# Performance work log

Measured on AMD Instinct MI355X. Metric: run time of the kernel, lower is better.

Reference implementation:

```python
import jax, jax.numpy as jnp
import numpy as np


def setup_inputs() -> dict:
    key = jax.random.key(0)
    B, U, I, H = 8192, 16, 128, 128
    k = jax.random.split(key, 6)
    s = 1.0 / np.sqrt(H)  # PyTorch GRU init scale (uniform(-s, s)); use scaled normal for test data
    return {
        "inputs": jax.random.normal(k[0], (B, U, I), dtype=jnp.float32),
        "hidden": jax.random.normal(k[1], (B, U, H), dtype=jnp.float32),
        "w_ih": jax.random.normal(k[2], (U, 3 * H, I), dtype=jnp.float32) * s,
        "w_hh": jax.random.normal(k[3], (U, 3 * H, H), dtype=jnp.float32) * s,
        "b_ih": jax.random.normal(k[4], (U, 3 * H), dtype=jnp.float32) * s,
        "b_hh": jax.random.normal(k[5], (U, 3 * H), dtype=jnp.float32) * s,
    }


def reference(inputs, hidden, w_ih, w_hh, b_ih, b_hh):
    # Grouped single-step GRU: one independent GRU cell per unit u, batched via einsum.
    # PyTorch GRU gate order in the 3H dim: [reset, update, new].
    H = hidden.shape[-1]
    # gates_x[b,u,g] = sum_i inputs[b,u,i] * w_ih[u,g,i] + b_ih[u,g]
    gx = jnp.einsum("bui,ugi->bug", inputs, w_ih) + b_ih  # (B, U, 3H)
    gh = jnp.einsum("buh,ugh->bug", hidden, w_hh) + b_hh  # (B, U, 3H)
    xr, xz, xn = gx[..., :H], gx[..., H:2 * H], gx[..., 2 * H:]
    hr, hz, hn = gh[..., :H], gh[..., H:2 * H], gh[..., 2 * H:]
    r = jax.nn.sigmoid(xr + hr)
    z = jax.nn.sigmoid(xz + hz)
    n = jnp.tanh(xn + r * hn)
    return (1.0 - z) * n + z * hidden  # (B, U, H)
```

## Files before the change

### kernel.cpp

```cpp
#include <hip/hip_runtime.h>
#include <hip/hip_bf16.h>

typedef __attribute__((ext_vector_type(8))) short  short8;
typedef __attribute__((ext_vector_type(4))) float  floatx4;

#define UH   2048
#define XPAD 264

#define MFMA16(a,b,c) __builtin_amdgcn_mfma_f32_16x16x32_bf16(a, b, c, 0, 0, 0)

static __device__ __forceinline__ unsigned int pkbf16(float a, float b) {
    __hip_bfloat162 p = __float22bfloat162_rn(make_float2(a, b));
    return *(unsigned int*)&p;
}

__global__ __launch_bounds__(256) void prep(const float* __restrict__ w_ih,
                                            const float* __restrict__ w_hh,
                                            const float* __restrict__ b_ih,
                                            const float* __restrict__ b_hh,
                                            __hip_bfloat16* __restrict__ Wc,
                                            float* __restrict__ bias_c) {
    if (blockIdx.x < 768) {
        int t   = blockIdx.x * 256 + threadIdx.x;
        int k8  = t & 31;
        int row = t >> 5;
        int u   = row / 384;
        int g   = row - u * 384;
        int k   = k8 * 8;
        const float* src = (k < 128) ? (w_ih + (size_t)row * 128 + k)
                                     : (w_hh + (size_t)row * 128 + (k - 128));
        float4 v0 = ((const float4*)src)[0];
        float4 v1 = ((const float4*)src)[1];
        uint4 w;
        w.x = pkbf16(v0.x, v0.y);
        w.y = pkbf16(v0.z, v0.w);
        w.z = pkbf16(v1.x, v1.y);
        w.w = pkbf16(v1.z, v1.w);
        int gt = g >> 4, lr = g & 15;
        int s  = k8 >> 2, lq = k8 & 3;
        size_t off = (size_t)((u * 24 + gt) * 8 + s) * 512 + (lq * 16 + lr) * 8;
        *(uint4*)(Wc + off) = w;
    } else {
        int idx = (blockIdx.x - 768) * 256 + threadIdx.x;
        int u = idx >> 9;
        int g = idx & 511;
        float v;
        if (g < 256)       v = b_ih[u * 384 + g] + b_hh[u * 384 + g];
        else if (g < 384)  v = b_ih[u * 384 + g];
        else               v = b_hh[u * 384 + (g - 128)];
        bias_c[idx] = v;
    }
}

__global__ __launch_bounds__(512, 3) void gru_fused(
    const float* __restrict__ inputs, const float* __restrict__ hidden,
    const __hip_bfloat16* __restrict__ Wc, const float* __restrict__ bias_c,
    float* __restrict__ out)
{
    __shared__ __align__(16) __hip_bfloat16 Xs[64][XPAD];
    __shared__ float bs[512];

    const int bx  = blockIdx.x;
    const int u   = ((bx & 7) << 1) | ((bx >> 3) & 1);
    const int mt  = bx >> 4;
    const int b0  = mt * 64;
    const int tid = threadIdx.x;

    bs[tid] = bias_c[u * 512 + tid];

    const float* xbase = inputs + (size_t)b0 * UH + u * 128;
    const float* hbase = hidden + (size_t)b0 * UH + u * 128;
    #pragma unroll
    for (int i = 0; i < 8; ++i) {
        int f   = i * 512 + tid;
        int row = f >> 6;
        int col = (f & 63) * 4;
        const float* src = (col < 128) ? (xbase + (size_t)row * UH + col)
                                       : (hbase + (size_t)row * UH + (col - 128));
        float4 v = *(const float4*)src;
        uint2 w;
        w.x = pkbf16(v.x, v.y);
        w.y = pkbf16(v.z, v.w);
        *(uint2*)&Xs[row][col] = w;
    }
    __syncthreads();

    const int lane = tid & 63;
    const int wv   = tid >> 6;
    const int lr   = lane & 15;
    const int lq   = lane >> 4;

    floatx4 aR[4], aZ[4], aXN[4], aHN[4];
    #pragma unroll
    for (int m4 = 0; m4 < 4; ++m4) {
        aR[m4]  = (floatx4){0.f, 0.f, 0.f, 0.f};
        aZ[m4]  = (floatx4){0.f, 0.f, 0.f, 0.f};
        aXN[m4] = (floatx4){0.f, 0.f, 0.f, 0.f};
        aHN[m4] = (floatx4){0.f, 0.f, 0.f, 0.f};
    }

    const short* WgU = (const short*)Wc + (size_t)u * 98304 + lane * 8;

    #pragma unroll
    for (int s = 0; s < 8; ++s) {
        short8 aF[4];
        #pragma unroll
        for (int m4 = 0; m4 < 4; ++m4)
            aF[m4] = *(const short8*)((const short*)&Xs[m4 * 16 + lr][0] + s * 32 + lq * 8);

        short8 bR = *(const short8*)(WgU + (size_t)(wv * 8 + s) * 512);
        short8 bZ = *(const short8*)(WgU + (size_t)(64 + wv * 8 + s) * 512);
        short8 bN = *(const short8*)(WgU + (size_t)(128 + wv * 8 + s) * 512);

        #pragma unroll
        for (int m4 = 0; m4 < 4; ++m4) {
            aR[m4] = MFMA16(aF[m4], bR, aR[m4]);
            aZ[m4] = MFMA16(aF[m4], bZ, aZ[m4]);
            if (s < 4) aXN[m4] = MFMA16(aF[m4], bN, aXN[m4]);
            else       aHN[m4] = MFMA16(aF[m4], bN, aHN[m4]);
        }
    }

    const int c = wv * 16 + lr;
    const float br  = bs[c];
    const float bz  = bs[128 + c];
    const float bxn = bs[256 + c];
    const float bhn = bs[384 + c];
    float* obase = out + (size_t)b0 * UH + u * 128 + c;

    #pragma unroll
    for (int m4 = 0; m4 < 4; ++m4) {
        #pragma unroll
        for (int r = 0; r < 4; ++r) {
            const int m = m4 * 16 + lq * 4 + r;
            float rv = __builtin_amdgcn_rcpf(1.f + __expf(-(aR[m4][r] + br)));
            float zv = __builtin_amdgcn_rcpf(1.f + __expf(-(aZ[m4][r] + bz)));
            float npre = (aXN[m4][r] + bxn) + rv * (aHN[m4][r] + bhn);
            float nv = 2.f * __builtin_amdgcn_rcpf(1.f + __expf(-2.f * npre)) - 1.f;
            float hv = __bfloat162float(Xs[m][128 + c]);
            obase[(size_t)m * UH] = nv + zv * (hv - nv);
        }
    }
}


extern "C" void kernel_launch(void* const* d_in, const int* in_sizes, int n_in,
                              void* d_out, int out_size, void* d_ws, size_t ws_size,
                              hipStream_t stream) {
    const float* inputs = (const float*)d_in[0];
    const float* hidden = (const float*)d_in[1];
    const float* w_ih   = (const float*)d_in[2];
    const float* w_hh   = (const float*)d_in[3];
    const float* b_ih   = (const float*)d_in[4];
    const float* b_hh   = (const float*)d_in[5];
    float* out = (float*)d_out;

    __hip_bfloat16* Wc = (__hip_bfloat16*)d_ws;
    float* bias_c = (float*)((char*)d_ws + (size_t)16 * 384 * 256 * 2);

    prep<<<dim3(800), dim3(256), 0, stream>>>(w_ih, w_hh, b_ih, b_hh, Wc, bias_c);
    gru_fused<<<dim3(2048), dim3(512), 0, stream>>>(inputs, hidden, Wc, bias_c, out);
}
```

Before: 200.0 us.

## Make GRU kernel persistent over 8 batch tiles with register-held weights and double buffering

```diff
diff --git a/kernel.cpp b/kernel.cpp
--- a/kernel.cpp
+++ b/kernel.cpp
@@ -52,93 +52,118 @@
     }
 }
 
-__global__ __launch_bounds__(512, 3) void gru_fused(
+__global__ __launch_bounds__(512, 2) void gru_fused(
     const float* __restrict__ inputs, const float* __restrict__ hidden,
     const __hip_bfloat16* __restrict__ Wc, const float* __restrict__ bias_c,
     float* __restrict__ out)
 {
-    __shared__ __align__(16) __hip_bfloat16 Xs[64][XPAD];
-    __shared__ float bs[512];
+    __shared__ __align__(16) __hip_bfloat16 Xs[2][64][XPAD];
 
-    const int bx  = blockIdx.x;
-    const int u   = ((bx & 7) << 1) | ((bx >> 3) & 1);
-    const int mt  = bx >> 4;
-    const int b0  = mt * 64;
-    const int tid = threadIdx.x;
-
-    bs[tid] = bias_c[u * 512 + tid];
-
-    const float* xbase = inputs + (size_t)b0 * UH + u * 128;
-    const float* hbase = hidden + (size_t)b0 * UH + u * 128;
-    #pragma unroll
-    for (int i = 0; i < 8; ++i) {
-        int f   = i * 512 + tid;
-        int row = f >> 6;
-        int col = (f & 63) * 4;
-        const float* src = (col < 128) ? (xbase + (size_t)row * UH + col)
-                                       : (hbase + (size_t)row * UH + (col - 128));
-        float4 v = *(const float4*)src;
-        uint2 w;
-        w.x = pkbf16(v.x, v.y);
-        w.y = pkbf16(v.z, v.w);
-        *(uint2*)&Xs[row][col] = w;
-    }
-    __syncthreads();
-
+    const int bx   = blockIdx.x;
+    const int u    = ((bx & 7) << 1) | ((bx >> 3) & 1);
+    const int mt0  = (bx >> 4) * 8;
+    const int tid  = threadIdx.x;
     const int lane = tid & 63;
     const int wv   = tid >> 6;
     const int lr   = lane & 15;
     const int lq   = lane >> 4;
 
-    floatx4 aR[4], aZ[4], aXN[4], aHN[4];
+    const short* WgU = (const short*)Wc + (size_t)u * 98304 + lane * 8;
+    short8 fR[8], fZ[8], fN[8];
     #pragma unroll
-    for (int m4 = 0; m4 < 4; ++m4) {
-        aR[m4]  = (floatx4){0.f, 0.f, 0.f, 0.f};
-        aZ[m4]  = (floatx4){0.f, 0.f, 0.f, 0.f};
-        aXN[m4] = (floatx4){0.f, 0.f, 0.f, 0.f};
-        aHN[m4] = (floatx4){0.f, 0.f, 0.f, 0.f};
+    for (int s = 0; s < 8; ++s) {
+        fR[s] = *(const short8*)(WgU + (size_t)(       wv * 8 + s) * 512);
+        fZ[s] = *(const short8*)(WgU + (size_t)( 64 +  wv * 8 + s) * 512);
+        fN[s] = *(const short8*)(WgU + (size_t)(128 +  wv * 8 + s) * 512);
     }
 
-    const short* WgU = (const short*)Wc + (size_t)u * 98304 + lane * 8;
+    const int   c   = wv * 16 + lr;
+    const float br  = bias_c[u * 512 + c];
+    const float bz  = bias_c[u * 512 + 128 + c];
+    const float bxn = bias_c[u * 512 + 256 + c];
+    const float bhn = bias_c[u * 512 + 384 + c];
 
-    #pragma unroll
-    for (int s = 0; s < 8; ++s) {
-        short8 aF[4];
+    const int scol = (tid & 63) * 4;
+    const float* sbase = ((scol < 128) ? (inputs + scol)
+                                       : (hidden + (scol - 128)))
+                       + (size_t)u * 128;
+
+    float4 stg[8];
+
+    auto ISSUE = [&](int mt) {
+        const float* p = sbase + (size_t)(mt * 64 + wv) * UH;
         #pragma unroll
-        for (int m4 = 0; m4 < 4; ++m4)
-            aF[m4] = *(const short8*)((const short*)&Xs[m4 * 16 + lr][0] + s * 32 + lq * 8);
+        for (int i = 0; i < 8; ++i)
+            stg[i] = *(const float4*)(p + (size_t)(i * 8) * UH);
+    };
+    auto WRITE = [&](int buf) {
+        #pragma unroll
+        for (int i = 0; i < 8; ++i) {
+            uint2 w;
+            w.x = pkbf16(stg[i].x, stg[i].y);
+            w.y = pkbf16(stg[i].z, stg[i].w);
+            *(uint2*)&Xs[buf][i * 8 + wv][scol] = w;
+        }
+    };
+    auto BARRIER = [&]() {
+        asm volatile("s_waitcnt lgkmcnt(0)" ::: "memory");
+        __builtin_amdgcn_sched_barrier(0);
+        __builtin_amdgcn_s_barrier();
+        __builtin_amdgcn_sched_barrier(0);
+    };
 
-        short8 bR = *(const short8*)(WgU + (size_t)(wv * 8 + s) * 512);
-        short8 bZ = *(const short8*)(WgU + (size_t)(64 + wv * 8 + s) * 512);
-        short8 bN = *(const short8*)(WgU + (size_t)(128 + wv * 8 + s) * 512);
+    ISSUE(mt0 + 0);
+    WRITE(0);
+    ISSUE(mt0 + 1);
+    BARRIER();
 
+    #pragma unroll 1
+    for (int j = 0; j < 8; ++j) {
+        const int buf = j & 1;
+
+        floatx4 aR[4], aZ[4], aXN[4], aHN[4];
         #pragma unroll
         for (int m4 = 0; m4 < 4; ++m4) {
-            aR[m4] = MFMA16(aF[m4], bR, aR[m4]);
-            aZ[m4] = MFMA16(aF[m4], bZ, aZ[m4]);
-            if (s < 4) aXN[m4] = MFMA16(aF[m4], bN, aXN[m4]);
-            else       aHN[m4] = MFMA16(aF[m4], bN, aHN[m4]);
+            aR[m4]  = (floatx4){0.f, 0.f, 0.f, 0.f};
+            aZ[m4]  = (floatx4){0.f, 0.f, 0.f, 0.f};
+            aXN[m4] = (floatx4){0.f, 0.f, 0.f, 0.f};
+            aHN[m4] = (floatx4){0.f, 0.f, 0.f, 0.f};
         }
-    }
+        #pragma unroll
+        for (int s = 0; s < 8; ++s) {
+            short8 aF[4];
+            #pragma unroll
+            for (int m4 = 0; m4 < 4; ++m4)
+                aF[m4] = *(const short8*)((const short*)&Xs[buf][m4 * 16 + lr][0]
+                                          + s * 32 + lq * 8);
+            #pragma unroll
+            for (int m4 = 0; m4 < 4; ++m4) {
+                aR[m4] = MFMA16(aF[m4], fR[s], aR[m4]);
+                aZ[m4] = MFMA16(aF[m4], fZ[s], aZ[m4]);
+                if (s < 4) aXN[m4] = MFMA16(aF[m4], fN[s], aXN[m4]);
+                else       aHN[m4] = MFMA16(aF[m4], fN[s], aHN[m4]);
+            }
+        }
 
-    const int c = wv * 16 + lr;
-    const float br  = bs[c];
-    const float bz  = bs[128 + c];
-    const float bxn = bs[256 + c];
-    const float bhn = bs[384 + c];
-    float* obase = out + (size_t)b0 * UH + u * 128 + c;
+        float* obase = out + (size_t)(mt0 + j) * 64 * UH + u * 128 + c;
+        #pragma unroll
+        for (int m4 = 0; m4 < 4; ++m4) {
+            #pragma unroll
+            for (int r = 0; r < 4; ++r) {
+                const int m = m4 * 16 + lq * 4 + r;
+                float rv = __builtin_amdgcn_rcpf(1.f + __expf(-(aR[m4][r] + br)));
+                float zv = __builtin_amdgcn_rcpf(1.f + __expf(-(aZ[m4][r] + bz)));
+                float npre = (aXN[m4][r] + bxn) + rv * (aHN[m4][r] + bhn);
+                float nv = 2.f * __builtin_amdgcn_rcpf(1.f + __expf(-2.f * npre)) - 1.f;
+                float hv = __bfloat162float(Xs[buf][m][128 + c]);
+                obase[(size_t)m * UH] = nv + zv * (hv - nv);
+            }
+        }
 
-    #pragma unroll
-    for (int m4 = 0; m4 < 4; ++m4) {
-        #pragma unroll
-        for (int r = 0; r < 4; ++r) {
-            const int m = m4 * 16 + lq * 4 + r;
-            float rv = __builtin_amdgcn_rcpf(1.f + __expf(-(aR[m4][r] + br)));
-            float zv = __builtin_amdgcn_rcpf(1.f + __expf(-(aZ[m4][r] + bz)));
-            float npre = (aXN[m4][r] + bxn) + rv * (aHN[m4][r] + bhn);
-            float nv = 2.f * __builtin_amdgcn_rcpf(1.f + __expf(-2.f * npre)) - 1.f;
-            float hv = __bfloat162float(Xs[m][128 + c]);
-            obase[(size_t)m * UH] = nv + zv * (hv - nv);
+        if (j < 7) {
+            WRITE(buf ^ 1);
+            if (j < 6) ISSUE(mt0 + j + 2);
+            BARRIER();
         }
     }
 }
@@ -159,5 +184,5 @@
     float* bias_c = (float*)((char*)d_ws + (size_t)16 * 384 * 256 * 2);
 
     prep<<<dim3(800), dim3(256), 0, stream>>>(w_ih, w_hh, b_ih, b_hh, Wc, bias_c);
-    gru_fused<<<dim3(2048), dim3(512), 0, stream>>>(inputs, hidden, Wc, bias_c, out);
+    gru_fused<<<dim3(256), dim3(512), 0, stream>>>(inputs, hidden, Wc, bias_c, out);
 }
```

Result: no change. 200.3 us (+0.1%).
